# Kernel tuning notes

Hardware: AMD Instinct MI355X
Metric: run time of the kernel (lower is better)

The kernel has to match this reference:

```python
import jax, jax.numpy as jnp
import numpy as np

N_NODES = 50000
N_EDGES = 800000
IN_CH = 10
HID = 32
HEADS = 4
OUT_CH = 64
EDIM = 1
NEG_SLOPE = 0.2  # PyG GATv2Conv default
LN_EPS = 1e-5


def _glorot(key, shape):
    fan_in, fan_out = shape[0], shape[-1]
    lim = np.sqrt(6.0 / (fan_in + fan_out))
    return jax.random.uniform(key, shape, jnp.float32, -lim, lim)


def setup_inputs() -> dict:
    key = jax.random.key(0)
    ks = jax.random.split(key, 16)
    x = jax.random.normal(ks[0], (N_NODES, IN_CH), jnp.float32)
    edge_index = jax.random.randint(ks[1], (2, N_EDGES), 0, N_NODES, jnp.int64)
    edge_attr = jax.random.normal(ks[2], (N_EDGES, EDIM), jnp.float32)
    return {
        "x": x,
        "edge_attr": edge_attr,
        "W1l": _glorot(ks[3], (IN_CH, HEADS * HID)),
        "W1r": _glorot(ks[4], (IN_CH, HEADS * HID)),
        "W1e": _glorot(ks[5], (EDIM, HEADS * HID)),
        "att1": _glorot(ks[6], (HEADS, HID)),
        "b1": jnp.zeros((HEADS * HID,), jnp.float32),
        "ln1_g": jnp.ones((HEADS * HID,), jnp.float32),
        "ln1_b": jnp.zeros((HEADS * HID,), jnp.float32),
        "W2l": _glorot(ks[7], (HEADS * HID, OUT_CH)),
        "W2r": _glorot(ks[8], (HEADS * HID, OUT_CH)),
        "W2e": _glorot(ks[9], (EDIM, OUT_CH)),
        "att2": _glorot(ks[10], (1, OUT_CH)),
        "b2": jnp.zeros((OUT_CH,), jnp.float32),
        "ln2_g": jnp.ones((OUT_CH,), jnp.float32),
        "ln2_b": jnp.zeros((OUT_CH,), jnp.float32),
        "edge_index": edge_index,
    }


def gatv2_layer(x, src, dst, edge_attr, Wl, Wr, We, att, bias, heads, ch, concat):
    # GATv2: e_ij = att . leaky_relu(Wl x_i + Wr x_j + We e_ij), softmax over j->i
    n = x.shape[0]
    xl = (x @ Wl).reshape(n, heads, ch)          # target projection [N,H,C]
    xr = (x @ Wr).reshape(n, heads, ch)          # source projection [N,H,C]
    ee = (edge_attr @ We).reshape(-1, heads, ch)  # [E,H,C]
    e = jax.nn.leaky_relu(xl[dst] + xr[src] + ee, NEG_SLOPE)  # [E,H,C]
    logit = jnp.einsum('ehc,hc->eh', e, att)     # [E,H]
    m = jax.ops.segment_max(logit, dst, num_segments=n)       # [N,H]
    expv = jnp.exp(logit - m[dst])
    denom = jax.ops.segment_sum(expv, dst, num_segments=n)    # [N,H]
    alpha = expv / denom[dst]                                  # [E,H]
    out = jax.ops.segment_sum(alpha[:, :, None] * xr[src], dst, num_segments=n)  # [N,H,C]
    out = out.reshape(n, heads * ch) if concat else out.mean(axis=1)
    return out + bias


def layer_norm(h, g, b):
    mu = h.mean(axis=-1, keepdims=True)
    var = ((h - mu) ** 2).mean(axis=-1, keepdims=True)
    return (h - mu) * jax.lax.rsqrt(var + LN_EPS) * g + b


def reference(x, edge_attr, W1l, W1r, W1e, att1, b1, ln1_g, ln1_b,
              W2l, W2r, W2e, att2, b2, ln2_g, ln2_b, edge_index):
    src, dst = edge_index[0], edge_index[1]
    h = gatv2_layer(x, src, dst, edge_attr, W1l, W1r, W1e, att1, b1, HEADS, HID, True)
    h = jax.nn.elu(layer_norm(h, ln1_g, ln1_b))
    # dropout is identity in eval mode
    h = gatv2_layer(h, src, dst, edge_attr, W2l, W2r, W2e, att2, b2, 1, OUT_CH, False)
    h = jax.nn.elu(layer_norm(h, ln2_g, ln2_b))
    return h
```

## Files before the change

kernel.cpp:

```cpp
#include <hip/hip_runtime.h>
#include <math.h>

#define NN 50000
#define NE 800000
#define IN_CH 10
#define NEGS 0.2f
#define LNEPS 1e-5f
#define LOG2E 1.4426950408889634f
#define SCAN_E 1024
#define NB 49

__device__ __forceinline__ float red16g(float v) {
    v += __shfl_xor(v, 1);  v += __shfl_xor(v, 2);
    v += __shfl_xor(v, 4);  v += __shfl_xor(v, 8);
    return v;
}
__device__ __forceinline__ float red32g(float v) {
    v = red16g(v); v += __shfl_xor(v, 16);
    return v;
}

__device__ __forceinline__ unsigned pack_bf16(float a, float b) {
    unsigned ua = __float_as_uint(a);
    unsigned ub = __float_as_uint(b);
    ua = (ua + 0x7FFFu + ((ua >> 16) & 1u)) >> 16;
    ub = (ub + 0x7FFFu + ((ub >> 16) & 1u)) & 0xFFFF0000u;
    return ua | ub;
}
__device__ __forceinline__ float bf_lo(unsigned d) { return __uint_as_float(d << 16); }
__device__ __forceinline__ float bf_hi(unsigned d) { return __uint_as_float(d & 0xFFFF0000u); }


__global__ __launch_bounds__(256) void k_proj1(
    const float* __restrict__ x, const float* __restrict__ Wl,
    const float* __restrict__ Wr, float* __restrict__ xl, unsigned* __restrict__ xrb) {
    int lane = threadIdx.x & 63;
    int n = blockIdx.x * 4 + (threadIdx.x >> 6);
    if (n >= NN) return;
    int c0 = lane * 2;
    float al0 = 0.f, al1 = 0.f, ar0 = 0.f, ar1 = 0.f;
#pragma unroll
    for (int k = 0; k < IN_CH; ++k) {
        float xv = x[n * IN_CH + k];
        al0 = fmaf(xv, Wl[k * 128 + c0], al0);
        al1 = fmaf(xv, Wl[k * 128 + c0 + 1], al1);
        ar0 = fmaf(xv, Wr[k * 128 + c0], ar0);
        ar1 = fmaf(xv, Wr[k * 128 + c0 + 1], ar1);
    }
    *(float2*)&xl[(size_t)n * 128 + c0] = make_float2(al0, al1);
    xrb[(size_t)n * 64 + lane] = pack_bf16(ar0, ar1);
}

__global__ __launch_bounds__(256) void k_proj2(
    const float* __restrict__ h1, const float* __restrict__ Wl,
    const float* __restrict__ Wr, float* __restrict__ xl2, unsigned* __restrict__ xr2b) {
    __shared__ float sh_h[64][36];
    __shared__ float sh_w[32][128];
    int t = threadIdx.x;
    int cg = t & 15, ng = t >> 4;
    int c0 = cg * 8;
    int nb = blockIdx.x * 64;
    float acc[4][8];
#pragma unroll
    for (int j = 0; j < 4; ++j)
#pragma unroll
        for (int i = 0; i < 8; ++i) acc[j][i] = 0.f;

    for (int kc = 0; kc < 128; kc += 32) {
#pragma unroll
        for (int i = 0; i < 2; ++i) {
            int fi = t + i * 256;
            int nl = fi >> 3, kq = fi & 7;
            int n = nb + nl;
            float4 v = make_float4(0.f, 0.f, 0.f, 0.f);
            if (n < NN) v = *(const float4*)&h1[(size_t)n * 128 + kc + kq * 4];
            *(float4*)&sh_h[nl][kq * 4] = v;
        }
#pragma unroll
        for (int i = 0; i < 4; ++i) {
            int fi = t + i * 256;
            int kl = fi >> 5, col = (fi & 31) * 4;
            const float* src = (col < 64) ? &Wl[(size_t)(kc + kl) * 64 + col]
                                          : &Wr[(size_t)(kc + kl) * 64 + col - 64];
            *(float4*)&sh_w[kl][col] = *(const float4*)src;
        }
        __syncthreads();
#pragma unroll
        for (int kl = 0; kl < 32; kl += 4) {
            float4 hv[4];
#pragma unroll
            for (int j = 0; j < 4; ++j) hv[j] = *(const float4*)&sh_h[ng + j * 16][kl];
#pragma unroll
            for (int kk = 0; kk < 4; ++kk) {
                float4 wa = *(const float4*)&sh_w[kl + kk][c0];
                float4 wb = *(const float4*)&sh_w[kl + kk][c0 + 4];
#pragma unroll
                for (int j = 0; j < 4; ++j) {
                    float hs = kk == 0 ? hv[j].x : kk == 1 ? hv[j].y : kk == 2 ? hv[j].z : hv[j].w;
                    acc[j][0] = fmaf(hs, wa.x, acc[j][0]);
                    acc[j][1] = fmaf(hs, wa.y, acc[j][1]);
                    acc[j][2] = fmaf(hs, wa.z, acc[j][2]);
                    acc[j][3] = fmaf(hs, wa.w, acc[j][3]);
                    acc[j][4] = fmaf(hs, wb.x, acc[j][4]);
                    acc[j][5] = fmaf(hs, wb.y, acc[j][5]);
                    acc[j][6] = fmaf(hs, wb.z, acc[j][6]);
                    acc[j][7] = fmaf(hs, wb.w, acc[j][7]);
                }
            }
        }
        __syncthreads();
    }
    if (cg < 8) {
#pragma unroll
        for (int j = 0; j < 4; ++j) {
            int n = nb + ng + j * 16;
            if (n < NN) {
                *(float4*)&xl2[(size_t)n * 64 + c0] =
                    make_float4(acc[j][0], acc[j][1], acc[j][2], acc[j][3]);
                *(float4*)&xl2[(size_t)n * 64 + c0 + 4] =
                    make_float4(acc[j][4], acc[j][5], acc[j][6], acc[j][7]);
            }
        }
    } else {
        int cc = c0 - 64;
#pragma unroll
        for (int j = 0; j < 4; ++j) {
            int n = nb + ng + j * 16;
            if (n < NN) {
                uint4 pk;
                pk.x = pack_bf16(acc[j][0], acc[j][1]);
                pk.y = pack_bf16(acc[j][2], acc[j][3]);
                pk.z = pack_bf16(acc[j][4], acc[j][5]);
                pk.w = pack_bf16(acc[j][6], acc[j][7]);
                *(uint4*)&xr2b[(size_t)n * 32 + (cc >> 1)] = pk;
            }
        }
    }
}


__global__ __launch_bounds__(256) void k_rank(
    const int* __restrict__ ei, int* __restrict__ deg, int* __restrict__ rank) {
    int e0 = (blockIdx.x * 256 + threadIdx.x) * 4;
    if (e0 >= NE) return;
    int4 d4 = *(const int4*)(ei + NE + e0);
    int4 r;
    r.x = atomicAdd(&deg[d4.x], 1);
    r.y = atomicAdd(&deg[d4.y], 1);
    r.z = atomicAdd(&deg[d4.z], 1);
    r.w = atomicAdd(&deg[d4.w], 1);
    *(int4*)(rank + e0) = r;
}

__global__ __launch_bounds__(256) void k_scan_block(
    const int* __restrict__ deg, int* __restrict__ rowstart, int* __restrict__ partial) {
    __shared__ int sh[256];
    int t = threadIdx.x;
    int base = blockIdx.x * SCAN_E + t * 4;
    int d0 = 0, d1 = 0, d2 = 0, d3 = 0;
    if (base + 0 < NN) d0 = deg[base + 0];
    if (base + 1 < NN) d1 = deg[base + 1];
    if (base + 2 < NN) d2 = deg[base + 2];
    if (base + 3 < NN) d3 = deg[base + 3];
    int mysum = d0 + d1 + d2 + d3;
    sh[t] = mysum;
    __syncthreads();
    for (int off = 1; off < 256; off <<= 1) {
        int v = (t >= off) ? sh[t - off] : 0;
        __syncthreads();
        sh[t] += v;
        __syncthreads();
    }
    int ex = sh[t] - mysum;
    if (base + 0 < NN) rowstart[base + 0] = ex;
    if (base + 1 < NN) rowstart[base + 1] = ex + d0;
    if (base + 2 < NN) rowstart[base + 2] = ex + d0 + d1;
    if (base + 3 < NN) rowstart[base + 3] = ex + d0 + d1 + d2;
    if (t == 255) partial[blockIdx.x] = sh[255];
}

__global__ __launch_bounds__(256) void k_scan_add(
    const int* __restrict__ partial, int* __restrict__ rowstart) {
    __shared__ int off;
    int t = threadIdx.x, bI = blockIdx.x;
    if (t == 0) {
        int s = 0;
        for (int k = 0; k < bI; ++k) s += partial[k];
        off = s;
    }
    __syncthreads();
    int base = bI * SCAN_E + t * 4;
#pragma unroll
    for (int i = 0; i < 4; ++i) {
        int idx = base + i;
        if (idx < NN) rowstart[idx] += off;
    }
    if (bI == 0 && t == 0) rowstart[NN] = NE;
}

__global__ __launch_bounds__(256) void k_scatter(
    const int* __restrict__ ei, const float* __restrict__ ea,
    const int* __restrict__ rowstart, const int* __restrict__ rank,
    long long* __restrict__ cpack) {
    int e0 = (blockIdx.x * 256 + threadIdx.x) * 4;
    if (e0 >= NE) return;
    int4 d4 = *(const int4*)(ei + NE + e0);
    int4 s4 = *(const int4*)(ei + e0);
    float4 a4 = *(const float4*)(ea + e0);
    int4 r4 = *(const int4*)(rank + e0);
    int p0 = rowstart[d4.x] + r4.x;
    int p1 = rowstart[d4.y] + r4.y;
    int p2 = rowstart[d4.z] + r4.z;
    int p3 = rowstart[d4.w] + r4.w;
    cpack[p0] = ((long long)(unsigned)__float_as_int(a4.x) << 32) | (unsigned)s4.x;
    cpack[p1] = ((long long)(unsigned)__float_as_int(a4.y) << 32) | (unsigned)s4.y;
    cpack[p2] = ((long long)(unsigned)__float_as_int(a4.z) << 32) | (unsigned)s4.z;
    cpack[p3] = ((long long)(unsigned)__float_as_int(a4.w) << 32) | (unsigned)s4.w;
}


__device__ __forceinline__ void edge1_step(
    const int2* __restrict__ cpack, const uint2* __restrict__ xrb, int p, int l,
    const float4& xld, const float4& We4, const float4& at6, const float4& at4,
    float4& acc, float& den, bool tail, int pmax) {
    bool valid = !tail || (p <= pmax);
    int2 pk = cpack[valid ? p : pmax];
    float eav = __int_as_float(pk.y);
    uint2 dw = xrb[(size_t)pk.x * 32 + l];
    float x0 = bf_lo(dw.x), x1 = bf_hi(dw.x);
    float x2 = bf_lo(dw.y), x3 = bf_hi(dw.y);
    float u0 = fmaf(eav, We4.x, xld.x) + x0;
    float u1 = fmaf(eav, We4.y, xld.y) + x1;
    float u2 = fmaf(eav, We4.z, xld.z) + x2;
    float u3 = fmaf(eav, We4.w, xld.w) + x3;
    float dot = fmaf(at6.x, u0, at4.x * fabsf(u0));
    dot = fmaf(at6.y, u1, fmaf(at4.y, fabsf(u1), dot));
    dot = fmaf(at6.z, u2, fmaf(at4.z, fabsf(u2), dot));
    dot = fmaf(at6.w, u3, fmaf(at4.w, fabsf(u3), dot));
    dot += __shfl_xor(dot, 1);
    dot += __shfl_xor(dot, 2);
    dot += __shfl_xor(dot, 4);
    float el = exp2f(dot);
    if (tail && !valid) el = 0.f;
    den += el;
    acc.x = fmaf(el, x0, acc.x);
    acc.y = fmaf(el, x1, acc.y);
    acc.z = fmaf(el, x2, acc.z);
    acc.w = fmaf(el, x3, acc.w);
}

__global__ __launch_bounds__(256) void k_fused1(
    const int* __restrict__ rs, const int2* __restrict__ cpack,
    const float* __restrict__ xl, const uint2* __restrict__ xrb,
    const float* __restrict__ We, const float* __restrict__ att,
    const float* __restrict__ bias, const float* __restrict__ g,
    const float* __restrict__ b, float* __restrict__ h1) {
    int lane = threadIdx.x & 63;
    int n = blockIdx.x * 4 + (threadIdx.x >> 6);
    if (n >= NN) return;
    int half = lane >> 5;
    int l = lane & 31;
    int c0 = l * 4;
    float4 xld = *(const float4*)&xl[(size_t)n * 128 + c0];
    float4 We4 = *(const float4*)&We[c0];
    float4 atv = *(const float4*)&att[c0];
    float4 at6 = make_float4(atv.x * (0.6f * LOG2E), atv.y * (0.6f * LOG2E),
                             atv.z * (0.6f * LOG2E), atv.w * (0.6f * LOG2E));
    float4 at4 = make_float4(atv.x * (0.4f * LOG2E), atv.y * (0.4f * LOG2E),
                             atv.z * (0.4f * LOG2E), atv.w * (0.4f * LOG2E));
    int beg = rs[n], end = rs[n + 1];
    int cnt = end - beg;
    int pfull = beg + (cnt & ~7);
    float4 acc[2];
    acc[0] = make_float4(0.f, 0.f, 0.f, 0.f);
    acc[1] = make_float4(0.f, 0.f, 0.f, 0.f);
    float den[2] = {0.f, 0.f};
    for (int p0 = beg; p0 < pfull; p0 += 8) {
#pragma unroll
        for (int s = 0; s < 4; ++s)
            edge1_step(cpack, xrb, p0 + s * 2 + half, l, xld, We4, at6, at4,
                       acc[s & 1], den[s & 1], false, 0);
    }
    if (cnt & 7) {
#pragma unroll
        for (int s = 0; s < 4; ++s)
            edge1_step(cpack, xrb, pfull + s * 2 + half, l, xld, We4, at6, at4,
                       acc[s & 1], den[s & 1], true, end - 1);
    }
    float4 a4 = make_float4(acc[0].x + acc[1].x, acc[0].y + acc[1].y,
                            acc[0].z + acc[1].z, acc[0].w + acc[1].w);
    float den0 = den[0] + den[1];
    a4.x += __shfl_xor(a4.x, 32);
    a4.y += __shfl_xor(a4.y, 32);
    a4.z += __shfl_xor(a4.z, 32);
    a4.w += __shfl_xor(a4.w, 32);
    den0 += __shfl_xor(den0, 32);
    float inv = den0 > 0.f ? 1.f / den0 : 0.f;
    float4 bv = *(const float4*)&bias[c0];
    float a0 = a4.x * inv + bv.x;
    float a1 = a4.y * inv + bv.y;
    float a2 = a4.z * inv + bv.z;
    float a3 = a4.w * inv + bv.w;
    float mu = red32g(a0 + a1 + a2 + a3) * (1.f / 128.f);
    float d0 = a0 - mu, d1 = a1 - mu, d2 = a2 - mu, d3 = a3 - mu;
    float var = red32g(d0 * d0 + d1 * d1 + d2 * d2 + d3 * d3) * (1.f / 128.f);
    float rsq = rsqrtf(var + LNEPS);
    float4 gv = *(const float4*)&g[c0];
    float4 bb = *(const float4*)&b[c0];
    float o0 = d0 * rsq * gv.x + bb.x;
    float o1 = d1 * rsq * gv.y + bb.y;
    float o2 = d2 * rsq * gv.z + bb.z;
    float o3 = d3 * rsq * gv.w + bb.w;
    o0 = o0 > 0.f ? o0 : __expf(o0) - 1.f;
    o1 = o1 > 0.f ? o1 : __expf(o1) - 1.f;
    o2 = o2 > 0.f ? o2 : __expf(o2) - 1.f;
    o3 = o3 > 0.f ? o3 : __expf(o3) - 1.f;
    if (half == 0)
        *(float4*)&h1[(size_t)n * 128 + c0] = make_float4(o0, o1, o2, o3);
}

__device__ __forceinline__ void edge2_step(
    const int2* __restrict__ cpack, const uint2* __restrict__ xr2b, int p, int l,
    const float4& xld, const float4& We4, const float4& at6, const float4& at4,
    float4& acc, float& den, bool tail, int pmax) {
    bool valid = !tail || (p <= pmax);
    int2 pk = cpack[valid ? p : pmax];
    float eav = __int_as_float(pk.y);
    uint2 dw = xr2b[(size_t)pk.x * 16 + l];
    float x0 = bf_lo(dw.x), x1 = bf_hi(dw.x);
    float x2 = bf_lo(dw.y), x3 = bf_hi(dw.y);
    float u0 = fmaf(eav, We4.x, xld.x) + x0;
    float u1 = fmaf(eav, We4.y, xld.y) + x1;
    float u2 = fmaf(eav, We4.z, xld.z) + x2;
    float u3 = fmaf(eav, We4.w, xld.w) + x3;
    float dot = fmaf(at6.x, u0, at4.x * fabsf(u0));
    dot = fmaf(at6.y, u1, fmaf(at4.y, fabsf(u1), dot));
    dot = fmaf(at6.z, u2, fmaf(at4.z, fabsf(u2), dot));
    dot = fmaf(at6.w, u3, fmaf(at4.w, fabsf(u3), dot));
    dot += __shfl_xor(dot, 1);
    dot += __shfl_xor(dot, 2);
    dot += __shfl_xor(dot, 4);
    dot += __shfl_xor(dot, 8);
    float el = exp2f(dot);
    if (tail && !valid) el = 0.f;
    den += el;
    acc.x = fmaf(el, x0, acc.x);
    acc.y = fmaf(el, x1, acc.y);
    acc.z = fmaf(el, x2, acc.z);
    acc.w = fmaf(el, x3, acc.w);
}

__global__ __launch_bounds__(256) void k_fused2(
    const int* __restrict__ rs, const int2* __restrict__ cpack,
    const float* __restrict__ xl2, const uint2* __restrict__ xr2b,
    const float* __restrict__ We, const float* __restrict__ att,
    const float* __restrict__ bias, const float* __restrict__ g,
    const float* __restrict__ b, float* __restrict__ out) {
    int lane = threadIdx.x & 63;
    int n = blockIdx.x * 4 + (threadIdx.x >> 6);
    if (n >= NN) return;
    int grp = lane >> 4;
    int l = lane & 15;
    int c0 = l * 4;
    float4 xld = *(const float4*)&xl2[(size_t)n * 64 + c0];
    float4 We4 = *(const float4*)&We[c0];
    float4 atv = *(const float4*)&att[c0];
    float4 at6 = make_float4(atv.x * (0.6f * LOG2E), atv.y * (0.6f * LOG2E),
                             atv.z * (0.6f * LOG2E), atv.w * (0.6f * LOG2E));
    float4 at4 = make_float4(atv.x * (0.4f * LOG2E), atv.y * (0.4f * LOG2E),
                             atv.z * (0.4f * LOG2E), atv.w * (0.4f * LOG2E));
    int beg = rs[n], end = rs[n + 1];
    int cnt = end - beg;
    int pfull = beg + (cnt & ~7);
    float4 acc[2];
    acc[0] = make_float4(0.f, 0.f, 0.f, 0.f);
    acc[1] = make_float4(0.f, 0.f, 0.f, 0.f);
    float den[2] = {0.f, 0.f};
    for (int p0 = beg; p0 < pfull; p0 += 8) {
#pragma unroll
        for (int s = 0; s < 2; ++s)
            edge2_step(cpack, xr2b, p0 + s * 4 + grp, l, xld, We4, at6, at4,
                       acc[s], den[s], false, 0);
    }
    if (cnt & 7) {
#pragma unroll
        for (int s = 0; s < 2; ++s)
            edge2_step(cpack, xr2b, pfull + s * 4 + grp, l, xld, We4, at6, at4,
                       acc[s], den[s], true, end - 1);
    }
    float4 a4 = make_float4(acc[0].x + acc[1].x, acc[0].y + acc[1].y,
                            acc[0].z + acc[1].z, acc[0].w + acc[1].w);
    float den0 = den[0] + den[1];
    a4.x += __shfl_xor(a4.x, 16); a4.x += __shfl_xor(a4.x, 32);
    a4.y += __shfl_xor(a4.y, 16); a4.y += __shfl_xor(a4.y, 32);
    a4.z += __shfl_xor(a4.z, 16); a4.z += __shfl_xor(a4.z, 32);
    a4.w += __shfl_xor(a4.w, 16); a4.w += __shfl_xor(a4.w, 32);
    den0 += __shfl_xor(den0, 16); den0 += __shfl_xor(den0, 32);
    float inv = den0 > 0.f ? 1.f / den0 : 0.f;
    float4 bv = *(const float4*)&bias[c0];
    float a0 = a4.x * inv + bv.x;
    float a1 = a4.y * inv + bv.y;
    float a2 = a4.z * inv + bv.z;
    float a3 = a4.w * inv + bv.w;
    float mu = red16g(a0 + a1 + a2 + a3) * (1.f / 64.f);
    float d0 = a0 - mu, d1 = a1 - mu, d2 = a2 - mu, d3 = a3 - mu;
    float var = red16g(d0 * d0 + d1 * d1 + d2 * d2 + d3 * d3) * (1.f / 64.f);
    float rsq = rsqrtf(var + LNEPS);
    float4 gv = *(const float4*)&g[c0];
    float4 bb = *(const float4*)&b[c0];
    float o0 = d0 * rsq * gv.x + bb.x;
    float o1 = d1 * rsq * gv.y + bb.y;
    float o2 = d2 * rsq * gv.z + bb.z;
    float o3 = d3 * rsq * gv.w + bb.w;
    o0 = o0 > 0.f ? o0 : __expf(o0) - 1.f;
    o1 = o1 > 0.f ? o1 : __expf(o1) - 1.f;
    o2 = o2 > 0.f ? o2 : __expf(o2) - 1.f;
    o3 = o3 > 0.f ? o3 : __expf(o3) - 1.f;
    if (grp == 0)
        *(float4*)&out[(size_t)n * 64 + c0] = make_float4(o0, o1, o2, o3);
}

extern "C" void kernel_launch(void* const* d_in, const int* in_sizes, int n_in,
                              void* d_out, int out_size, void* d_ws, size_t ws_size,
                              hipStream_t stream) {
    const float* x    = (const float*)d_in[0];
    const float* ea   = (const float*)d_in[1];
    const float* W1l  = (const float*)d_in[2];
    const float* W1r  = (const float*)d_in[3];
    const float* W1e  = (const float*)d_in[4];
    const float* att1 = (const float*)d_in[5];
    const float* b1   = (const float*)d_in[6];
    const float* ln1g = (const float*)d_in[7];
    const float* ln1b = (const float*)d_in[8];
    const float* W2l  = (const float*)d_in[9];
    const float* W2r  = (const float*)d_in[10];
    const float* W2e  = (const float*)d_in[11];
    const float* att2 = (const float*)d_in[12];
    const float* b2   = (const float*)d_in[13];
    const float* ln2g = (const float*)d_in[14];
    const float* ln2b = (const float*)d_in[15];
    const int*   ei   = (const int*)d_in[16];
    float* out = (float*)d_out;
    float* ws  = (float*)d_ws;

    const size_t A = (size_t)NN * 128;
    float* xl1 = ws;
    float* h1  = ws + A;
    float* xl2 = ws + 2 * A;
    unsigned* xr1b = (unsigned*)(ws + 2 * A + (size_t)NN * 64);
    unsigned* xr2b = xr1b + (size_t)NN * 64;
    long long* cpack = (long long*)(xr2b + (size_t)NN * 32);
    int* rank    = (int*)(cpack + (size_t)NE);
    int* deg     = rank + NE;
    int* rowstart= deg + NN;
    int* partial = rowstart + NN + 1;

    hipMemsetAsync(deg, 0, NN * sizeof(int), stream);

    k_proj1<<<(NN + 3) / 4, 256, 0, stream>>>(x, W1l, W1r, xl1, xr1b);
    k_rank<<<(NE / 4 + 255) / 256, 256, 0, stream>>>(ei, deg, rank);
    k_scan_block<<<NB, 256, 0, stream>>>(deg, rowstart, partial);
    k_scan_add<<<NB, 256, 0, stream>>>(partial, rowstart);
    k_scatter<<<(NE / 4 + 255) / 256, 256, 0, stream>>>(ei, ea, rowstart, rank, cpack);

    k_fused1<<<(NN + 3) / 4, 256, 0, stream>>>(rowstart, (const int2*)cpack, xl1,
                                               (const uint2*)xr1b, W1e, att1, b1,
                                               ln1g, ln1b, h1);
    k_proj2<<<(NN + 63) / 64, 256, 0, stream>>>(h1, W2l, W2r, xl2, xr2b);
    k_fused2<<<(NN + 3) / 4, 256, 0, stream>>>(rowstart, (const int2*)cpack, xl2,
                                               (const uint2*)xr2b, W2e, att2, b2,
                                               ln2g, ln2b, out);
}
```

Before: 301.0 us.

## Merge proj1 with degree ranking, single-block scan, packed FMA edge loops

Layer-1 projection and the atomic degree/rank pass now run as one launch by splitting the block range. The two-kernel scan becomes a single 1024-thread block scan. The edge loops use 2-wide float vector FMAs and 32-bit unsigned byte-offset addressing for the bf16 gathers. This removes two kernel launches and aims to cut VALU instruction count in the hot edge loops, at the cost of a serial single-block scan with strided per-thread reads.

Result: slower. 382.0 us (+26.9%).

```diff
diff --git a/kernel.cpp b/kernel.cpp
--- a/kernel.cpp
+++ b/kernel.cpp
@@ -7,9 +7,15 @@
 #define NEGS 0.2f
 #define LNEPS 1e-5f
 #define LOG2E 1.4426950408889634f
-#define SCAN_E 1024
-#define NB 49
-
+#define P1_BLOCKS 12500
+#define RK_BLOCKS 782
+#define SCAN_C 49
+
+typedef float f2 __attribute__((ext_vector_type(2)));
+
+__device__ __forceinline__ f2 pkfma(f2 a, f2 b, f2 c) {
+    return __builtin_elementwise_fma(a, b, c);
+}
 __device__ __forceinline__ float red16g(float v) {
     v += __shfl_xor(v, 1);  v += __shfl_xor(v, 2);
     v += __shfl_xor(v, 4);  v += __shfl_xor(v, 8);
@@ -30,172 +36,65 @@
 __device__ __forceinline__ float bf_lo(unsigned d) { return __uint_as_float(d << 16); }
 __device__ __forceinline__ float bf_hi(unsigned d) { return __uint_as_float(d & 0xFFFF0000u); }
 
-
-__global__ __launch_bounds__(256) void k_proj1(
+__global__ __launch_bounds__(256) void k_proj1_rank(
     const float* __restrict__ x, const float* __restrict__ Wl,
-    const float* __restrict__ Wr, float* __restrict__ xl, unsigned* __restrict__ xrb) {
-    int lane = threadIdx.x & 63;
-    int n = blockIdx.x * 4 + (threadIdx.x >> 6);
-    if (n >= NN) return;
-    int c0 = lane * 2;
-    float al0 = 0.f, al1 = 0.f, ar0 = 0.f, ar1 = 0.f;
-#pragma unroll
-    for (int k = 0; k < IN_CH; ++k) {
-        float xv = x[n * IN_CH + k];
-        al0 = fmaf(xv, Wl[k * 128 + c0], al0);
-        al1 = fmaf(xv, Wl[k * 128 + c0 + 1], al1);
-        ar0 = fmaf(xv, Wr[k * 128 + c0], ar0);
-        ar1 = fmaf(xv, Wr[k * 128 + c0 + 1], ar1);
-    }
-    *(float2*)&xl[(size_t)n * 128 + c0] = make_float2(al0, al1);
-    xrb[(size_t)n * 64 + lane] = pack_bf16(ar0, ar1);
-}
-
-__global__ __launch_bounds__(256) void k_proj2(
-    const float* __restrict__ h1, const float* __restrict__ Wl,
-    const float* __restrict__ Wr, float* __restrict__ xl2, unsigned* __restrict__ xr2b) {
-    __shared__ float sh_h[64][36];
-    __shared__ float sh_w[32][128];
+    const float* __restrict__ Wr, float* __restrict__ xl, unsigned* __restrict__ xrb,
+    const int* __restrict__ ei, int* __restrict__ deg, int* __restrict__ rank) {
+    int bI = blockIdx.x;
+    if (bI < P1_BLOCKS) {
+        int lane = threadIdx.x & 63;
+        int n = bI * 4 + (threadIdx.x >> 6);
+        int c0 = lane * 2;
+        float al0 = 0.f, al1 = 0.f, ar0 = 0.f, ar1 = 0.f;
+#pragma unroll
+        for (int k = 0; k < IN_CH; ++k) {
+            float xv = x[n * IN_CH + k];
+            al0 = fmaf(xv, Wl[k * 128 + c0], al0);
+            al1 = fmaf(xv, Wl[k * 128 + c0 + 1], al1);
+            ar0 = fmaf(xv, Wr[k * 128 + c0], ar0);
+            ar1 = fmaf(xv, Wr[k * 128 + c0 + 1], ar1);
+        }
+        *(float2*)&xl[(size_t)n * 128 + c0] = make_float2(al0, al1);
+        xrb[(size_t)n * 64 + lane] = pack_bf16(ar0, ar1);
+    } else {
+        int e0 = ((bI - P1_BLOCKS) * 256 + threadIdx.x) * 4;
+        if (e0 >= NE) return;
+        int4 d4 = *(const int4*)(ei + NE + e0);
+        int4 r;
+        r.x = atomicAdd(&deg[d4.x], 1);
+        r.y = atomicAdd(&deg[d4.y], 1);
+        r.z = atomicAdd(&deg[d4.z], 1);
+        r.w = atomicAdd(&deg[d4.w], 1);
+        *(int4*)(rank + e0) = r;
+    }
+}
+
+__global__ __launch_bounds__(1024) void k_scan(
+    const int* __restrict__ deg, int* __restrict__ rowstart) {
+    __shared__ int sh[1024];
     int t = threadIdx.x;
-    int cg = t & 15, ng = t >> 4;
-    int c0 = cg * 8;
-    int nb = blockIdx.x * 64;
-    float acc[4][8];
-#pragma unroll
-    for (int j = 0; j < 4; ++j)
-#pragma unroll
-        for (int i = 0; i < 8; ++i) acc[j][i] = 0.f;
-
-    for (int kc = 0; kc < 128; kc += 32) {
-#pragma unroll
-        for (int i = 0; i < 2; ++i) {
-            int fi = t + i * 256;
-            int nl = fi >> 3, kq = fi & 7;
-            int n = nb + nl;
-            float4 v = make_float4(0.f, 0.f, 0.f, 0.f);
-            if (n < NN) v = *(const float4*)&h1[(size_t)n * 128 + kc + kq * 4];
-            *(float4*)&sh_h[nl][kq * 4] = v;
-        }
-#pragma unroll
-        for (int i = 0; i < 4; ++i) {
-            int fi = t + i * 256;
-            int kl = fi >> 5, col = (fi & 31) * 4;
-            const float* src = (col < 64) ? &Wl[(size_t)(kc + kl) * 64 + col]
-                                          : &Wr[(size_t)(kc + kl) * 64 + col - 64];
-            *(float4*)&sh_w[kl][col] = *(const float4*)src;
-        }
-        __syncthreads();
-#pragma unroll
-        for (int kl = 0; kl < 32; kl += 4) {
-            float4 hv[4];
-#pragma unroll
-            for (int j = 0; j < 4; ++j) hv[j] = *(const float4*)&sh_h[ng + j * 16][kl];
-#pragma unroll
-            for (int kk = 0; kk < 4; ++kk) {
-                float4 wa = *(const float4*)&sh_w[kl + kk][c0];
-                float4 wb = *(const float4*)&sh_w[kl + kk][c0 + 4];
-#pragma unroll
-                for (int j = 0; j < 4; ++j) {
-                    float hs = kk == 0 ? hv[j].x : kk == 1 ? hv[j].y : kk == 2 ? hv[j].z : hv[j].w;
-                    acc[j][0] = fmaf(hs, wa.x, acc[j][0]);
-                    acc[j][1] = fmaf(hs, wa.y, acc[j][1]);
-                    acc[j][2] = fmaf(hs, wa.z, acc[j][2]);
-                    acc[j][3] = fmaf(hs, wa.w, acc[j][3]);
-                    acc[j][4] = fmaf(hs, wb.x, acc[j][4]);
-                    acc[j][5] = fmaf(hs, wb.y, acc[j][5]);
-                    acc[j][6] = fmaf(hs, wb.z, acc[j][6]);
-                    acc[j][7] = fmaf(hs, wb.w, acc[j][7]);
-                }
-            }
-        }
-        __syncthreads();
-    }
-    if (cg < 8) {
-#pragma unroll
-        for (int j = 0; j < 4; ++j) {
-            int n = nb + ng + j * 16;
-            if (n < NN) {
-                *(float4*)&xl2[(size_t)n * 64 + c0] =
-                    make_float4(acc[j][0], acc[j][1], acc[j][2], acc[j][3]);
-                *(float4*)&xl2[(size_t)n * 64 + c0 + 4] =
-                    make_float4(acc[j][4], acc[j][5], acc[j][6], acc[j][7]);
-            }
-        }
-    } else {
-        int cc = c0 - 64;
-#pragma unroll
-        for (int j = 0; j < 4; ++j) {
-            int n = nb + ng + j * 16;
-            if (n < NN) {
-                uint4 pk;
-                pk.x = pack_bf16(acc[j][0], acc[j][1]);
-                pk.y = pack_bf16(acc[j][2], acc[j][3]);
-                pk.z = pack_bf16(acc[j][4], acc[j][5]);
-                pk.w = pack_bf16(acc[j][6], acc[j][7]);
-                *(uint4*)&xr2b[(size_t)n * 32 + (cc >> 1)] = pk;
-            }
-        }
-    }
-}
-
-
-__global__ __launch_bounds__(256) void k_rank(
-    const int* __restrict__ ei, int* __restrict__ deg, int* __restrict__ rank) {
-    int e0 = (blockIdx.x * 256 + threadIdx.x) * 4;
-    if (e0 >= NE) return;
-    int4 d4 = *(const int4*)(ei + NE + e0);
-    int4 r;
-    r.x = atomicAdd(&deg[d4.x], 1);
-    r.y = atomicAdd(&deg[d4.y], 1);
-    r.z = atomicAdd(&deg[d4.z], 1);
-    r.w = atomicAdd(&deg[d4.w], 1);
-    *(int4*)(rank + e0) = r;
-}
-
-__global__ __launch_bounds__(256) void k_scan_block(
-    const int* __restrict__ deg, int* __restrict__ rowstart, int* __restrict__ partial) {
-    __shared__ int sh[256];
-    int t = threadIdx.x;
-    int base = blockIdx.x * SCAN_E + t * 4;
-    int d0 = 0, d1 = 0, d2 = 0, d3 = 0;
-    if (base + 0 < NN) d0 = deg[base + 0];
-    if (base + 1 < NN) d1 = deg[base + 1];
-    if (base + 2 < NN) d2 = deg[base + 2];
-    if (base + 3 < NN) d3 = deg[base + 3];
-    int mysum = d0 + d1 + d2 + d3;
-    sh[t] = mysum;
+    int base = t * SCAN_C;
+    int sum = 0;
+#pragma unroll
+    for (int i = 0; i < SCAN_C; ++i) {
+        int idx = base + i;
+        if (idx < NN) sum += deg[idx];
+    }
+    sh[t] = sum;
     __syncthreads();
-    for (int off = 1; off < 256; off <<= 1) {
+    for (int off = 1; off < 1024; off <<= 1) {
         int v = (t >= off) ? sh[t - off] : 0;
         __syncthreads();
         sh[t] += v;
         __syncthreads();
     }
-    int ex = sh[t] - mysum;
-    if (base + 0 < NN) rowstart[base + 0] = ex;
-    if (base + 1 < NN) rowstart[base + 1] = ex + d0;
-    if (base + 2 < NN) rowstart[base + 2] = ex + d0 + d1;
-    if (base + 3 < NN) rowstart[base + 3] = ex + d0 + d1 + d2;
-    if (t == 255) partial[blockIdx.x] = sh[255];
-}
-
-__global__ __launch_bounds__(256) void k_scan_add(
-    const int* __restrict__ partial, int* __restrict__ rowstart) {
-    __shared__ int off;
-    int t = threadIdx.x, bI = blockIdx.x;
-    if (t == 0) {
-        int s = 0;
-        for (int k = 0; k < bI; ++k) s += partial[k];
-        off = s;
-    }
-    __syncthreads();
-    int base = bI * SCAN_E + t * 4;
-#pragma unroll
-    for (int i = 0; i < 4; ++i) {
+    int run = sh[t] - sum;
+#pragma unroll
+    for (int i = 0; i < SCAN_C; ++i) {
         int idx = base + i;
-        if (idx < NN) rowstart[idx] += off;
-    }
-    if (bI == 0 && t == 0) rowstart[NN] = NE;
+        if (idx < NN) { rowstart[idx] = run; run += deg[idx]; }
+    }
+    if (t == 0) rowstart[NN] = NE;
 }
 
 __global__ __launch_bounds__(256) void k_scatter(
@@ -218,40 +117,128 @@
     cpack[p3] = ((long long)(unsigned)__float_as_int(a4.w) << 32) | (unsigned)s4.w;
 }
 
+__global__ __launch_bounds__(256) void k_proj2(
+    const float* __restrict__ h1, const float* __restrict__ Wl,
+    const float* __restrict__ Wr, float* __restrict__ xl2, unsigned* __restrict__ xr2b) {
+    __shared__ float sh_h[64][36];
+    __shared__ float sh_w[32][128];
+    int t = threadIdx.x;
+    int cg = t & 15, ng = t >> 4;
+    int c0 = cg * 8;
+    int nb = blockIdx.x * 64;
+    float acc[4][8];
+#pragma unroll
+    for (int j = 0; j < 4; ++j)
+#pragma unroll
+        for (int i = 0; i < 8; ++i) acc[j][i] = 0.f;
+
+    for (int kc = 0; kc < 128; kc += 32) {
+#pragma unroll
+        for (int i = 0; i < 2; ++i) {
+            int fi = t + i * 256;
+            int nl = fi >> 3, kq = fi & 7;
+            int n = nb + nl;
+            float4 v = make_float4(0.f, 0.f, 0.f, 0.f);
+            if (n < NN) v = *(const float4*)&h1[(size_t)n * 128 + kc + kq * 4];
+            *(float4*)&sh_h[nl][kq * 4] = v;
+        }
+#pragma unroll
+        for (int i = 0; i < 4; ++i) {
+            int fi = t + i * 256;
+            int kl = fi >> 5, col = (fi & 31) * 4;
+            const float* src = (col < 64) ? &Wl[(size_t)(kc + kl) * 64 + col]
+                                          : &Wr[(size_t)(kc + kl) * 64 + col - 64];
+            *(float4*)&sh_w[kl][col] = *(const float4*)src;
+        }
+        __syncthreads();
+#pragma unroll
+        for (int kl = 0; kl < 32; kl += 4) {
+            float4 hv[4];
+#pragma unroll
+            for (int j = 0; j < 4; ++j) hv[j] = *(const float4*)&sh_h[ng + j * 16][kl];
+#pragma unroll
+            for (int kk = 0; kk < 4; ++kk) {
+                float4 wa = *(const float4*)&sh_w[kl + kk][c0];
+                float4 wb = *(const float4*)&sh_w[kl + kk][c0 + 4];
+#pragma unroll
+                for (int j = 0; j < 4; ++j) {
+                    float hs = kk == 0 ? hv[j].x : kk == 1 ? hv[j].y : kk == 2 ? hv[j].z : hv[j].w;
+                    acc[j][0] = fmaf(hs, wa.x, acc[j][0]);
+                    acc[j][1] = fmaf(hs, wa.y, acc[j][1]);
+                    acc[j][2] = fmaf(hs, wa.z, acc[j][2]);
+                    acc[j][3] = fmaf(hs, wa.w, acc[j][3]);
+                    acc[j][4] = fmaf(hs, wb.x, acc[j][4]);
+                    acc[j][5] = fmaf(hs, wb.y, acc[j][5]);
+                    acc[j][6] = fmaf(hs, wb.z, acc[j][6]);
+                    acc[j][7] = fmaf(hs, wb.w, acc[j][7]);
+                }
+            }
+        }
+        __syncthreads();
+    }
+    if (cg < 8) {
+#pragma unroll
+        for (int j = 0; j < 4; ++j) {
+            int n = nb + ng + j * 16;
+            if (n < NN) {
+                *(float4*)&xl2[(size_t)n * 64 + c0] =
+                    make_float4(acc[j][0], acc[j][1], acc[j][2], acc[j][3]);
+                *(float4*)&xl2[(size_t)n * 64 + c0 + 4] =
+                    make_float4(acc[j][4], acc[j][5], acc[j][6], acc[j][7]);
+            }
+        }
+    } else {
+        int cc = c0 - 64;
+#pragma unroll
+        for (int j = 0; j < 4; ++j) {
+            int n = nb + ng + j * 16;
+            if (n < NN) {
+                uint4 pk;
+                pk.x = pack_bf16(acc[j][0], acc[j][1]);
+                pk.y = pack_bf16(acc[j][2], acc[j][3]);
+                pk.z = pack_bf16(acc[j][4], acc[j][5]);
+                pk.w = pack_bf16(acc[j][6], acc[j][7]);
+                *(uint4*)&xr2b[(size_t)n * 32 + (cc >> 1)] = pk;
+            }
+        }
+    }
+}
+
 
 __device__ __forceinline__ void edge1_step(
-    const int2* __restrict__ cpack, const uint2* __restrict__ xrb, int p, int l,
-    const float4& xld, const float4& We4, const float4& at6, const float4& at4,
-    float4& acc, float& den, bool tail, int pmax) {
+    const int2* __restrict__ cpack, const unsigned char* __restrict__ xrb, int p, int l,
+    const f2& xl01, const f2& xl23, const f2& We01, const f2& We23,
+    const f2& at6a, const f2& at6b, const f2& at4a, const f2& at4b,
+    f2& acc01, f2& acc23, float& den, bool tail, int pmax) {
     bool valid = !tail || (p <= pmax);
     int2 pk = cpack[valid ? p : pmax];
     float eav = __int_as_float(pk.y);
-    uint2 dw = xrb[(size_t)pk.x * 32 + l];
-    float x0 = bf_lo(dw.x), x1 = bf_hi(dw.x);
-    float x2 = bf_lo(dw.y), x3 = bf_hi(dw.y);
-    float u0 = fmaf(eav, We4.x, xld.x) + x0;
-    float u1 = fmaf(eav, We4.y, xld.y) + x1;
-    float u2 = fmaf(eav, We4.z, xld.z) + x2;
-    float u3 = fmaf(eav, We4.w, xld.w) + x3;
-    float dot = fmaf(at6.x, u0, at4.x * fabsf(u0));
-    dot = fmaf(at6.y, u1, fmaf(at4.y, fabsf(u1), dot));
-    dot = fmaf(at6.z, u2, fmaf(at4.z, fabsf(u2), dot));
-    dot = fmaf(at6.w, u3, fmaf(at4.w, fabsf(u3), dot));
+    unsigned off = (unsigned)pk.x * 256u + (unsigned)(l * 8);
+    uint2 dw = *(const uint2*)(xrb + off);
+    f2 x01, x23;
+    x01.x = bf_lo(dw.x); x01.y = bf_hi(dw.x);
+    x23.x = bf_lo(dw.y); x23.y = bf_hi(dw.y);
+    f2 ev = {eav, eav};
+    f2 u01 = pkfma(ev, We01, xl01) + x01;
+    f2 u23 = pkfma(ev, We23, xl23) + x23;
+    float dot = fmaf(at6a.x, u01.x, at4a.x * fabsf(u01.x));
+    dot = fmaf(at6a.y, u01.y, fmaf(at4a.y, fabsf(u01.y), dot));
+    dot = fmaf(at6b.x, u23.x, fmaf(at4b.x, fabsf(u23.x), dot));
+    dot = fmaf(at6b.y, u23.y, fmaf(at4b.y, fabsf(u23.y), dot));
     dot += __shfl_xor(dot, 1);
     dot += __shfl_xor(dot, 2);
     dot += __shfl_xor(dot, 4);
     float el = exp2f(dot);
     if (tail && !valid) el = 0.f;
     den += el;
-    acc.x = fmaf(el, x0, acc.x);
-    acc.y = fmaf(el, x1, acc.y);
-    acc.z = fmaf(el, x2, acc.z);
-    acc.w = fmaf(el, x3, acc.w);
+    f2 el2 = {el, el};
+    acc01 = pkfma(el2, x01, acc01);
+    acc23 = pkfma(el2, x23, acc23);
 }
 
 __global__ __launch_bounds__(256) void k_fused1(
     const int* __restrict__ rs, const int2* __restrict__ cpack,
-    const float* __restrict__ xl, const uint2* __restrict__ xrb,
+    const float* __restrict__ xl, const unsigned char* __restrict__ xrb,
     const float* __restrict__ We, const float* __restrict__ att,
     const float* __restrict__ bias, const float* __restrict__ g,
     const float* __restrict__ b, float* __restrict__ h1) {
@@ -261,46 +248,49 @@
     int half = lane >> 5;
     int l = lane & 31;
     int c0 = l * 4;
-    float4 xld = *(const float4*)&xl[(size_t)n * 128 + c0];
-    float4 We4 = *(const float4*)&We[c0];
+    float4 xldf = *(const float4*)&xl[(size_t)n * 128 + c0];
+    float4 Wef = *(const float4*)&We[c0];
     float4 atv = *(const float4*)&att[c0];
-    float4 at6 = make_float4(atv.x * (0.6f * LOG2E), atv.y * (0.6f * LOG2E),
-                             atv.z * (0.6f * LOG2E), atv.w * (0.6f * LOG2E));
-    float4 at4 = make_float4(atv.x * (0.4f * LOG2E), atv.y * (0.4f * LOG2E),
-                             atv.z * (0.4f * LOG2E), atv.w * (0.4f * LOG2E));
+    f2 xl01 = {xldf.x, xldf.y}, xl23 = {xldf.z, xldf.w};
+    f2 We01 = {Wef.x, Wef.y}, We23 = {Wef.z, Wef.w};
+    f2 at6a = {atv.x * (0.6f * LOG2E), atv.y * (0.6f * LOG2E)};
+    f2 at6b = {atv.z * (0.6f * LOG2E), atv.w * (0.6f * LOG2E)};
+    f2 at4a = {atv.x * (0.4f * LOG2E), atv.y * (0.4f * LOG2E)};
+    f2 at4b = {atv.z * (0.4f * LOG2E), atv.w * (0.4f * LOG2E)};
     int beg = rs[n], end = rs[n + 1];
     int cnt = end - beg;
     int pfull = beg + (cnt & ~7);
-    float4 acc[2];
-    acc[0] = make_float4(0.f, 0.f, 0.f, 0.f);
-    acc[1] = make_float4(0.f, 0.f, 0.f, 0.f);
+    f2 a01[2] = {{0.f, 0.f}, {0.f, 0.f}};
+    f2 a23[2] = {{0.f, 0.f}, {0.f, 0.f}};
     float den[2] = {0.f, 0.f};
     for (int p0 = beg; p0 < pfull; p0 += 8) {
 #pragma unroll
         for (int s = 0; s < 4; ++s)
-            edge1_step(cpack, xrb, p0 + s * 2 + half, l, xld, We4, at6, at4,
-                       acc[s & 1], den[s & 1], false, 0);
+            edge1_step(cpack, xrb, p0 + s * 2 + half, l, xl01, xl23, We01, We23,
+                       at6a, at6b, at4a, at4b, a01[s & 1], a23[s & 1], den[s & 1],
+                       false, 0);
     }
     if (cnt & 7) {
 #pragma unroll
         for (int s = 0; s < 4; ++s)
-            edge1_step(cpack, xrb, pfull + s * 2 + half, l, xld, We4, at6, at4,
-                       acc[s & 1], den[s & 1], true, end - 1);
-    }
-    float4 a4 = make_float4(acc[0].x + acc[1].x, acc[0].y + acc[1].y,
-                            acc[0].z + acc[1].z, acc[0].w + acc[1].w);
+            edge1_step(cpack, xrb, pfull + s * 2 + half, l, xl01, xl23, We01, We23,
+                       at6a, at6b, at4a, at4b, a01[s & 1], a23[s & 1], den[s & 1],
+                       true, end - 1);
+    }
+    f2 s01 = a01[0] + a01[1];
+    f2 s23 = a23[0] + a23[1];
     float den0 = den[0] + den[1];
-    a4.x += __shfl_xor(a4.x, 32);
-    a4.y += __shfl_xor(a4.y, 32);
-    a4.z += __shfl_xor(a4.z, 32);
-    a4.w += __shfl_xor(a4.w, 32);
+    s01.x += __shfl_xor(s01.x, 32);
+    s01.y += __shfl_xor(s01.y, 32);
+    s23.x += __shfl_xor(s23.x, 32);
+    s23.y += __shfl_xor(s23.y, 32);
     den0 += __shfl_xor(den0, 32);
     float inv = den0 > 0.f ? 1.f / den0 : 0.f;
     float4 bv = *(const float4*)&bias[c0];
-    float a0 = a4.x * inv + bv.x;
-    float a1 = a4.y * inv + bv.y;
-    float a2 = a4.z * inv + bv.z;
-    float a3 = a4.w * inv + bv.w;
+    float a0 = s01.x * inv + bv.x;
+    float a1 = s01.y * inv + bv.y;
+    float a2 = s23.x * inv + bv.z;
+    float a3 = s23.y * inv + bv.w;
     float mu = red32g(a0 + a1 + a2 + a3) * (1.f / 128.f);
     float d0 = a0 - mu, d1 = a1 - mu, d2 = a2 - mu, d3 = a3 - mu;
     float var = red32g(d0 * d0 + d1 * d1 + d2 * d2 + d3 * d3) * (1.f / 128.f);
@@ -320,23 +310,25 @@
 }
 
 __device__ __forceinline__ void edge2_step(
-    const int2* __restrict__ cpack, const uint2* __restrict__ xr2b, int p, int l,
-    const float4& xld, const float4& We4, const float4& at6, const float4& at4,
-    float4& acc, float& den, bool tail, int pmax) {
+    const int2* __restrict__ cpack, const unsigned char* __restrict__ xr2b, int p, int l,
+    const f2& xl01, const f2& xl23, const f2& We01, const f2& We23,
+    const f2& at6a, const f2& at6b, const f2& at4a, const f2& at4b,
+    f2& acc01, f2& acc23, float& den, bool tail, int pmax) {
     bool valid = !tail || (p <= pmax);
     int2 pk = cpack[valid ? p : pmax];
     float eav = __int_as_float(pk.y);
-    uint2 dw = xr2b[(size_t)pk.x * 16 + l];
-    float x0 = bf_lo(dw.x), x1 = bf_hi(dw.x);
-    float x2 = bf_lo(dw.y), x3 = bf_hi(dw.y);
-    float u0 = fmaf(eav, We4.x, xld.x) + x0;
-    float u1 = fmaf(eav, We4.y, xld.y) + x1;
-    float u2 = fmaf(eav, We4.z, xld.z) + x2;
-    float u3 = fmaf(eav, We4.w, xld.w) + x3;
-    float dot = fmaf(at6.x, u0, at4.x * fabsf(u0));
-    dot = fmaf(at6.y, u1, fmaf(at4.y, fabsf(u1), dot));
-    dot = fmaf(at6.z, u2, fmaf(at4.z, fabsf(u2), dot));
-    dot = fmaf(at6.w, u3, fmaf(at4.w, fabsf(u3), dot));
+    unsigned off = (unsigned)pk.x * 128u + (unsigned)(l * 8);
+    uint2 dw = *(const uint2*)(xr2b + off);
+    f2 x01, x23;
+    x01.x = bf_lo(dw.x); x01.y = bf_hi(dw.x);
+    x23.x = bf_lo(dw.y); x23.y = bf_hi(dw.y);
+    f2 ev = {eav, eav};
+    f2 u01 = pkfma(ev, We01, xl01) + x01;
+    f2 u23 = pkfma(ev, We23, xl23) + x23;
+    float dot = fmaf(at6a.x, u01.x, at4a.x * fabsf(u01.x));
+    dot = fmaf(at6a.y, u01.y, fmaf(at4a.y, fabsf(u01.y), dot));
+    dot = fmaf(at6b.x, u23.x, fmaf(at4b.x, fabsf(u23.x), dot));
+    dot = fmaf(at6b.y, u23.y, fmaf(at4b.y, fabsf(u23.y), dot));
     dot += __shfl_xor(dot, 1);
     dot += __shfl_xor(dot, 2);
     dot += __shfl_xor(dot, 4);
@@ -344,15 +336,14 @@
     float el = exp2f(dot);
     if (tail && !valid) el = 0.f;
     den += el;
-    acc.x = fmaf(el, x0, acc.x);
-    acc.y = fmaf(el, x1, acc.y);
-    acc.z = fmaf(el, x2, acc.z);
-    acc.w = fmaf(el, x3, acc.w);
+    f2 el2 = {el, el};
+    acc01 = pkfma(el2, x01, acc01);
+    acc23 = pkfma(el2, x23, acc23);
 }
 
 __global__ __launch_bounds__(256) void k_fused2(
     const int* __restrict__ rs, const int2* __restrict__ cpack,
-    const float* __restrict__ xl2, const uint2* __restrict__ xr2b,
+    const float* __restrict__ xl2, const unsigned char* __restrict__ xr2b,
     const float* __restrict__ We, const float* __restrict__ att,
     const float* __restrict__ bias, const float* __restrict__ g,
     const float* __restrict__ b, float* __restrict__ out) {
@@ -362,46 +353,47 @@
     int grp = lane >> 4;
     int l = lane & 15;
     int c0 = l * 4;
-    float4 xld = *(const float4*)&xl2[(size_t)n * 64 + c0];
-    float4 We4 = *(const float4*)&We[c0];
+    float4 xldf = *(const float4*)&xl2[(size_t)n * 64 + c0];
+    float4 Wef = *(const float4*)&We[c0];
     float4 atv = *(const float4*)&att[c0];
-    float4 at6 = make_float4(atv.x * (0.6f * LOG2E), atv.y * (0.6f * LOG2E),
-                             atv.z * (0.6f * LOG2E), atv.w * (0.6f * LOG2E));
-    float4 at4 = make_float4(atv.x * (0.4f * LOG2E), atv.y * (0.4f * LOG2E),
-                             atv.z * (0.4f * LOG2E), atv.w * (0.4f * LOG2E));
+    f2 xl01 = {xldf.x, xldf.y}, xl23 = {xldf.z, xldf.w};
+    f2 We01 = {Wef.x, Wef.y}, We23 = {Wef.z, Wef.w};
+    f2 at6a = {atv.x * (0.6f * LOG2E), atv.y * (0.6f * LOG2E)};
+    f2 at6b = {atv.z * (0.6f * LOG2E), atv.w * (0.6f * LOG2E)};
+    f2 at4a = {atv.x * (0.4f * LOG2E), atv.y * (0.4f * LOG2E)};
+    f2 at4b = {atv.z * (0.4f * LOG2E), atv.w * (0.4f * LOG2E)};
     int beg = rs[n], end = rs[n + 1];
     int cnt = end - beg;
     int pfull = beg + (cnt & ~7);
-    float4 acc[2];
-    acc[0] = make_float4(0.f, 0.f, 0.f, 0.f);
-    acc[1] = make_float4(0.f, 0.f, 0.f, 0.f);
+    f2 a01[2] = {{0.f, 0.f}, {0.f, 0.f}};
+    f2 a23[2] = {{0.f, 0.f}, {0.f, 0.f}};
     float den[2] = {0.f, 0.f};
     for (int p0 = beg; p0 < pfull; p0 += 8) {
 #pragma unroll
         for (int s = 0; s < 2; ++s)
-            edge2_step(cpack, xr2b, p0 + s * 4 + grp, l, xld, We4, at6, at4,
-                       acc[s], den[s], false, 0);
+            edge2_step(cpack, xr2b, p0 + s * 4 + grp, l, xl01, xl23, We01, We23,
+                       at6a, at6b, at4a, at4b, a01[s], a23[s], den[s], false, 0);
     }
     if (cnt & 7) {
 #pragma unroll
         for (int s = 0; s < 2; ++s)
-            edge2_step(cpack, xr2b, pfull + s * 4 + grp, l, xld, We4, at6, at4,
-                       acc[s], den[s], true, end - 1);
-    }
-    float4 a4 = make_float4(acc[0].x + acc[1].x, acc[0].y + acc[1].y,
-                            acc[0].z + acc[1].z, acc[0].w + acc[1].w);
+            edge2_step(cpack, xr2b, pfull + s * 4 + grp, l, xl01, xl23, We01, We23,
+                       at6a, at6b, at4a, at4b, a01[s], a23[s], den[s], true, end - 1);
+    }
+    f2 s01 = a01[0] + a01[1];
+    f2 s23 = a23[0] + a23[1];
     float den0 = den[0] + den[1];
-    a4.x += __shfl_xor(a4.x, 16); a4.x += __shfl_xor(a4.x, 32);
-    a4.y += __shfl_xor(a4.y, 16); a4.y += __shfl_xor(a4.y, 32);
-    a4.z += __shfl_xor(a4.z, 16); a4.z += __shfl_xor(a4.z, 32);
-    a4.w += __shfl_xor(a4.w, 16); a4.w += __shfl_xor(a4.w, 32);
+    s01.x += __shfl_xor(s01.x, 16); s01.x += __shfl_xor(s01.x, 32);
+    s01.y += __shfl_xor(s01.y, 16); s01.y += __shfl_xor(s01.y, 32);
+    s23.x += __shfl_xor(s23.x, 16); s23.x += __shfl_xor(s23.x, 32);
+    s23.y += __shfl_xor(s23.y, 16); s23.y += __shfl_xor(s23.y, 32);
     den0 += __shfl_xor(den0, 16); den0 += __shfl_xor(den0, 32);
     float inv = den0 > 0.f ? 1.f / den0 : 0.f;
     float4 bv = *(const float4*)&bias[c0];
-    float a0 = a4.x * inv + bv.x;
-    float a1 = a4.y * inv + bv.y;
-    float a2 = a4.z * inv + bv.z;
-    float a3 = a4.w * inv + bv.w;
+    float a0 = s01.x * inv + bv.x;
+    float a1 = s01.y * inv + bv.y;
+    float a2 = s23.x * inv + bv.z;
+    float a3 = s23.y * inv + bv.w;
     float mu = red16g(a0 + a1 + a2 + a3) * (1.f / 64.f);
     float d0 = a0 - mu, d1 = a1 - mu, d2 = a2 - mu, d3 = a3 - mu;
     float var = red16g(d0 * d0 + d1 * d1 + d2 * d2 + d3 * d3) * (1.f / 64.f);
@@ -453,21 +445,19 @@
     int* rank    = (int*)(cpack + (size_t)NE);
     int* deg     = rank + NE;
     int* rowstart= deg + NN;
-    int* partial = rowstart + NN + 1;
 
     hipMemsetAsync(deg, 0, NN * sizeof(int), stream);
 
-    k_proj1<<<(NN + 3) / 4, 256, 0, stream>>>(x, W1l, W1r, xl1, xr1b);
-    k_rank<<<(NE / 4 + 255) / 256, 256, 0, stream>>>(ei, deg, rank);
-    k_scan_block<<<NB, 256, 0, stream>>>(deg, rowstart, partial);
-    k_scan_add<<<NB, 256, 0, stream>>>(partial, rowstart);
+    k_proj1_rank<<<P1_BLOCKS + RK_BLOCKS, 256, 0, stream>>>(x, W1l, W1r, xl1, xr1b,
+                                                            ei, deg, rank);
+    k_scan<<<1, 1024, 0, stream>>>(deg, rowstart);
     k_scatter<<<(NE / 4 + 255) / 256, 256, 0, stream>>>(ei, ea, rowstart, rank, cpack);
 
     k_fused1<<<(NN + 3) / 4, 256, 0, stream>>>(rowstart, (const int2*)cpack, xl1,
-                                               (const uint2*)xr1b, W1e, att1, b1,
+                                               (const unsigned char*)xr1b, W1e, att1, b1,
                                                ln1g, ln1b, h1);
     k_proj2<<<(NN + 63) / 64, 256, 0, stream>>>(h1, W2l, W2r, xl2, xr2b);
     k_fused2<<<(NN + 3) / 4, 256, 0, stream>>>(rowstart, (const int2*)cpack, xl2,
-                                               (const uint2*)xr2b, W2e, att2, b2,
+                                               (const unsigned char*)xr2b, W2e, att2, b2,
                                                ln2g, ln2b, out);
 }
```
